# Performance work log

Measured on AMD Instinct MI355X. Metric: run time of the kernel, lower is better.

Reference implementation:

```python
import jax, jax.numpy as jnp
import numpy as np

N_EMBD = 2048
NUM_GROUPS = 8
EXPERTS_PER_GROUP = 8
ROUTER_TEMPERATURE = 1.0
N_TOKENS = 16384


def setup_inputs() -> dict:
    key = jax.random.key(0)
    kx, kg, ke = jax.random.split(key, 3)
    x = jax.random.normal(kx, (N_TOKENS, N_EMBD), dtype=jnp.float32)
    # nn.Linear(in, out, bias=False) stores weight as [out, in]; kaiming-uniform-ish scale
    bound = 1.0 / np.sqrt(N_EMBD)
    group_gate_w = jax.random.uniform(kg, (NUM_GROUPS, N_EMBD), dtype=jnp.float32,
                                      minval=-bound, maxval=bound)
    expert_gate_w = jax.random.uniform(ke, (NUM_GROUPS * EXPERTS_PER_GROUP, N_EMBD),
                                       dtype=jnp.float32, minval=-bound, maxval=bound)
    return {"x": x, "group_gate_w": group_gate_w, "expert_gate_w": expert_gate_w}


def reference(x, group_gate_w, expert_gate_w):
    N = x.shape[0]
    G = NUM_GROUPS
    E_g = EXPERTS_PER_GROUP
    inv_temp = 1.0 / ROUTER_TEMPERATURE

    # Level 1: group routing
    group_logits = jnp.einsum('nd,gd->ng', x, group_gate_w)            # [N, G]
    group_probs = jax.nn.softmax(group_logits * inv_temp, axis=-1)     # [N, G]
    group_mask = group_probs >= (1.0 / G)                              # [N, G]

    # Level 2: expert routing within each group
    expert_logits = jnp.einsum('nd,ed->ne', x, expert_gate_w)          # [N, G*E_g]
    expert_logits = expert_logits.reshape(N, G, E_g)
    expert_probs = jax.nn.softmax(expert_logits * inv_temp, axis=-1)   # [N, G, E_g]
    expert_mask = expert_probs >= (1.0 / E_g)                          # [N, G, E_g]

    valid_mask_3d = group_mask[:, :, None] & expert_mask               # [N, G, E_g]
    selected_weights_3d = (group_probs[:, :, None] * expert_probs) * valid_mask_3d.astype(x.dtype)

    valid_mask = valid_mask_3d.reshape(N, G * E_g)
    selected_weights = selected_weights_3d.reshape(N, G * E_g)
    weight_sum = jnp.clip(jnp.sum(selected_weights, axis=-1, keepdims=True), 1e-9, None)
    normalized_weights = selected_weights / weight_sum
    return (valid_mask, normalized_weights)
```

## Files before the change

### kernel.cpp

```cpp
#include <hip/hip_runtime.h>


#define NT 16384
#define NE 2048
#define NCHUNK 16
#define TOK 32
#define NTH 256
#define TILE 2048
#define BUFSZ 40960
#define LDS_BYTES 81920

typedef _Float16 v8h __attribute__((ext_vector_type(8)));
typedef float    v4f __attribute__((ext_vector_type(4)));

__global__ __launch_bounds__(NTH, 2)
void router(const float* __restrict__ x, const float* __restrict__ gw,
            const float* __restrict__ ew, float* __restrict__ out)
{
    __shared__ __align__(16) char sm[LDS_BYTES];
    const int tid  = threadIdx.x;
    const int lane = tid & 63;
    const int w    = tid >> 6;
    const int t0   = blockIdx.x * TOK;

    const float* wsrc[5]; int who[5]; int wz[5];
    #pragma unroll
    for (int i = 0; i < 5; ++i) {
        int s = tid + i * NTH;
        int gate = s >> 4, kslot = s & 15;
        int ks = kslot >> 2, q = kslot & 3;
        int m = gate & 15, g = gate >> 4;
        int swz = (q ^ (ks << 1)) & 7;
        who[i] = (g * 4 + ks) * TILE + (((q * 16 + m) ^ swz) << 4);
        if (gate < 64)      { wz[i] = 0; wsrc[i] = ew + (size_t)gate * NE + kslot * 8; }
        else if (gate < 72) { wz[i] = 0; wsrc[i] = gw + (size_t)(gate - 64) * NE + kslot * 8; }
        else                { wz[i] = 1; wsrc[i] = ew; }
    }

    const int tt = w >> 1, s2 = w & 1;
    const float* xp = x + (size_t)(t0 + tt * 16 + (lane & 15)) * NE + (lane >> 4) * 8;

    int rdk[2];
    #pragma unroll
    for (int ksl = 0; ksl < 2; ++ksl) {
        int ks = s2 * 2 + ksl;
        int swz = ((lane >> 4) ^ (ks << 1)) & 7;
        rdk[ksl] = ks * TILE + ((lane ^ swz) << 4);
    }

    float4 wr[5][2], xr[2][2];

    auto wload = [&](int c) {
        const int kc = c * 128;
        #pragma unroll
        for (int i = 0; i < 5; ++i) {
            if (!wz[i]) {
                wr[i][0] = *(const float4*)(wsrc[i] + kc);
                wr[i][1] = *(const float4*)(wsrc[i] + kc + 4);
            } else {
                wr[i][0] = make_float4(0.f, 0.f, 0.f, 0.f);
                wr[i][1] = make_float4(0.f, 0.f, 0.f, 0.f);
            }
        }
    };
    auto xload = [&](int c) {
        #pragma unroll
        for (int ksl = 0; ksl < 2; ++ksl) {
            const float* p = xp + c * 128 + (s2 * 2 + ksl) * 32;
            xr[ksl][0] = *(const float4*)(p);
            xr[ksl][1] = *(const float4*)(p + 4);
        }
    };
    auto split8 = [](const float4& a, const float4& b, v8h& h, v8h& l) {
        float v[8] = {a.x, a.y, a.z, a.w, b.x, b.y, b.z, b.w};
        #pragma unroll
        for (int j = 0; j < 8; ++j) {
            _Float16 hh = (_Float16)v[j];
            h[j] = hh;
            l[j] = (_Float16)((v[j] - (float)hh) * 2048.0f);
        }
    };
    auto wcommit = [&](int buf) {
        const int bb = buf * BUFSZ;
        #pragma unroll
        for (int i = 0; i < 5; ++i) {
            v8h h, l;
            split8(wr[i][0], wr[i][1], h, l);
            *(v8h*)(sm + bb + who[i])        = h;
            *(v8h*)(sm + bb + who[i] + 1024) = l;
        }
    };

    v4f accHH[5], accC[5];
    #pragma unroll
    for (int g = 0; g < 5; ++g) { accHH[g] = (v4f)(0.f); accC[g] = (v4f)(0.f); }

    wload(0); xload(0);
    wcommit(0);
    v8h Bh[2], Bl[2];
    for (int c = 0; c < NCHUNK; ++c) {
        #pragma unroll
        for (int ksl = 0; ksl < 2; ++ksl)
            split8(xr[ksl][0], xr[ksl][1], Bh[ksl], Bl[ksl]);
        if (c + 1 < NCHUNK) { xload(c + 1); wload(c + 1); }
        __syncthreads();
        const int bb = (c & 1) * BUFSZ;
        #pragma unroll
        for (int ksl = 0; ksl < 2; ++ksl) {
            #pragma unroll
            for (int g = 0; g < 5; ++g) {
                const char* ab = sm + bb + g * (4 * TILE) + rdk[ksl];
                v8h Ah = *(const v8h*)(ab);
                v8h Al = *(const v8h*)(ab + 1024);
                accHH[g] = __builtin_amdgcn_mfma_f32_16x16x32_f16(Ah, Bh[ksl], accHH[g], 0, 0, 0);
                accC[g]  = __builtin_amdgcn_mfma_f32_16x16x32_f16(Ah, Bl[ksl], accC[g], 0, 0, 0);
                accC[g]  = __builtin_amdgcn_mfma_f32_16x16x32_f16(Al, Bh[ksl], accC[g], 0, 0, 0);
            }
        }
        if (c + 1 < NCHUNK) wcommit((c + 1) & 1);
    }
    __syncthreads();

    float part[5][4];
    #pragma unroll
    for (int g = 0; g < 5; ++g)
        #pragma unroll
        for (int r = 0; r < 4; ++r)
            part[g][r] = accHH[g][r] + accC[g][r] * (1.0f / 2048.0f);

    float* red = (float*)sm;
    if (s2 == 1) {
        #pragma unroll
        for (int g = 0; g < 5; ++g)
            #pragma unroll
            for (int r = 0; r < 4; ++r)
                red[((tt * 5 + g) * 4 + r) * 64 + lane] = part[g][r];
    }
    __syncthreads();
    float* la = (float*)(sm + 10240);
    if (s2 == 0) {
        #pragma unroll
        for (int g = 0; g < 5; ++g)
            #pragma unroll
            for (int r = 0; r < 4; ++r) {
                float v = part[g][r] + red[((tt * 5 + g) * 4 + r) * 64 + lane];
                int gate  = g * 16 + (lane >> 4) * 4 + r;
                int token = tt * 16 + (lane & 15);
                la[token * 84 + gate] = v;
            }
    }
    __syncthreads();

    if (lane < 8) {
        const int token = w * 8 + lane;
        const float* lg = la + token * 84;
        float* M  = (float*)(sm + 20992) + token * 64;
        float* Wn = (float*)(sm + 29184) + token * 64;

        float gpb[8];
        float gmax = lg[64];
        #pragma unroll
        for (int g = 1; g < 8; ++g) gmax = fmaxf(gmax, lg[64 + g]);
        float gsum = 0.f;
        #pragma unroll
        for (int g = 0; g < 8; ++g) { gpb[g] = __expf(lg[64 + g] - gmax); gsum += gpb[g]; }
        const float ginv = 1.f / gsum;

        float sel[64];
        float wsum = 0.f;
        #pragma unroll
        for (int g = 0; g < 8; ++g) {
            const float gp_ = gpb[g] * ginv;
            float emax = lg[g * 8];
            #pragma unroll
            for (int j = 1; j < 8; ++j) emax = fmaxf(emax, lg[g * 8 + j]);
            float ep[8]; float esum = 0.f;
            #pragma unroll
            for (int j = 0; j < 8; ++j) { ep[j] = __expf(lg[g * 8 + j] - emax); esum += ep[j]; }
            const float einv = 1.f / esum;
            const bool gm = gp_ >= 0.125f;
            #pragma unroll
            for (int j = 0; j < 8; ++j) {
                const float pe = ep[j] * einv;
                const bool v = gm && (pe >= 0.125f);
                const float ww = v ? gp_ * pe : 0.f;
                M[g * 8 + j] = v ? 1.f : 0.f;
                sel[g * 8 + j] = ww;
                wsum += ww;
            }
        }
        const float inv = 1.f / fmaxf(wsum, 1e-9f);
        #pragma unroll
        for (int e = 0; e < 64; ++e) Wn[e] = sel[e] * inv;
    }
    __syncthreads();

    const float4* M4 = (const float4*)(sm + 20992);
    const float4* W4 = (const float4*)(sm + 29184);
    float4* o0 = (float4*)(out + (size_t)t0 * 64);
    float4* o1 = (float4*)(out + (size_t)NT * 64 + (size_t)t0 * 64);
    o0[tid]       = M4[tid];
    o0[tid + 256] = M4[tid + 256];
    o1[tid]       = W4[tid];
    o1[tid + 256] = W4[tid + 256];
}

extern "C" void kernel_launch(void* const* d_in, const int* in_sizes, int n_in,
                              void* d_out, int out_size, void* d_ws, size_t ws_size,
                              hipStream_t stream) {
    const float* x  = (const float*)d_in[0];
    const float* gw = (const float*)d_in[1];
    const float* ew = (const float*)d_in[2];
    float* out = (float*)d_out;
    (void)d_ws; (void)ws_size;

    router<<<dim3(NT / TOK), dim3(NTH), 0, stream>>>(x, gw, ew, out);
}
```

Baseline: 209.8 us.

## Pre-split gate weights to fp16 hi/lo in workspace and read them directly

Adds a prep kernel that converts the gate weights once per call into pre-swizzled fp16 hi/lo arrays in the workspace. The router then reads those fragments straight from global/L2 instead of staging them through double-buffered LDS with per-block conversion. The token tile is halved to 16 so 1024 blocks run, and all four waves split K, followed by a 4-way reduction. This removes the per-block weight conversion, the LDS traffic and the per-chunk barriers, at the cost of an extra launch and more repeated L2 reads of the weights.

```diff
diff --git a/kernel.cpp b/kernel.cpp
--- a/kernel.cpp
+++ b/kernel.cpp
@@ -3,159 +3,120 @@
 
 #define NT 16384
 #define NE 2048
-#define NCHUNK 16
-#define TOK 32
 #define NTH 256
-#define TILE 2048
-#define BUFSZ 40960
-#define LDS_BYTES 81920
+#define NBLK 1024
+#define WS_HALFS 163840
 
 typedef _Float16 v8h __attribute__((ext_vector_type(8)));
 typedef float    v4f __attribute__((ext_vector_type(4)));
 
-__global__ __launch_bounds__(NTH, 2)
-void router(const float* __restrict__ x, const float* __restrict__ gw,
-            const float* __restrict__ ew, float* __restrict__ out)
+__global__ __launch_bounds__(256, 1)
+void prep(const float* __restrict__ gw, const float* __restrict__ ew,
+          _Float16* __restrict__ wf)
 {
-    __shared__ __align__(16) char sm[LDS_BYTES];
+    const int f = blockIdx.x * 256 + threadIdx.x;
+    const int j  = f & 7;
+    const int sl = (f >> 3) & 63;
+    const int ks = (f >> 9) & 63;
+    const int g  = f >> 15;
+    const int q  = sl >> 4, m = sl & 15;
+    const int gate = g * 16 + m;
+    const int k = ks * 32 + q * 8 + j;
+    float v = 0.f;
+    if (gate < 64)      v = ew[gate * NE + k];
+    else if (gate < 72) v = gw[(gate - 64) * NE + k];
+    const _Float16 h = (_Float16)v;
+    wf[f]            = h;
+    wf[WS_HALFS + f] = (_Float16)((v - (float)h) * 2048.0f);
+}
+
+__global__ __launch_bounds__(NTH, 4)
+void router(const float* __restrict__ x, const _Float16* __restrict__ wf,
+            float* __restrict__ out)
+{
+    __shared__ __align__(16) char sm[20736];
     const int tid  = threadIdx.x;
     const int lane = tid & 63;
     const int w    = tid >> 6;
-    const int t0   = blockIdx.x * TOK;
+    const int t0   = blockIdx.x * 16;
 
-    const float* wsrc[5]; int who[5]; int wz[5];
+    const float* xp = x + (size_t)(t0 + (lane & 15)) * NE + (lane >> 4) * 8;
+
+    v4f accH[5], accC[5];
     #pragma unroll
-    for (int i = 0; i < 5; ++i) {
-        int s = tid + i * NTH;
-        int gate = s >> 4, kslot = s & 15;
-        int ks = kslot >> 2, q = kslot & 3;
-        int m = gate & 15, g = gate >> 4;
-        int swz = (q ^ (ks << 1)) & 7;
-        who[i] = (g * 4 + ks) * TILE + (((q * 16 + m) ^ swz) << 4);
-        if (gate < 64)      { wz[i] = 0; wsrc[i] = ew + (size_t)gate * NE + kslot * 8; }
-        else if (gate < 72) { wz[i] = 0; wsrc[i] = gw + (size_t)(gate - 64) * NE + kslot * 8; }
-        else                { wz[i] = 1; wsrc[i] = ew; }
-    }
+    for (int g = 0; g < 5; ++g) { accH[g] = (v4f)(0.f); accC[g] = (v4f)(0.f); }
 
-    const int tt = w >> 1, s2 = w & 1;
-    const float* xp = x + (size_t)(t0 + tt * 16 + (lane & 15)) * NE + (lane >> 4) * 8;
+    float4 xr0, xr1;
+    auto xload = [&](int s) {
+        const float* p = xp + (size_t)(w * 16 + s) * 32;
+        xr0 = *(const float4*)(p);
+        xr1 = *(const float4*)(p + 4);
+    };
 
-    int rdk[2];
-    #pragma unroll
-    for (int ksl = 0; ksl < 2; ++ksl) {
-        int ks = s2 * 2 + ksl;
-        int swz = ((lane >> 4) ^ (ks << 1)) & 7;
-        rdk[ksl] = ks * TILE + ((lane ^ swz) << 4);
-    }
-
-    float4 wr[5][2], xr[2][2];
-
-    auto wload = [&](int c) {
-        const int kc = c * 128;
-        #pragma unroll
-        for (int i = 0; i < 5; ++i) {
-            if (!wz[i]) {
-                wr[i][0] = *(const float4*)(wsrc[i] + kc);
-                wr[i][1] = *(const float4*)(wsrc[i] + kc + 4);
-            } else {
-                wr[i][0] = make_float4(0.f, 0.f, 0.f, 0.f);
-                wr[i][1] = make_float4(0.f, 0.f, 0.f, 0.f);
+    xload(0);
+    for (int s = 0; s < 16; ++s) {
+        v8h Bh, Bl;
+        {
+            const float xv[8] = {xr0.x, xr0.y, xr0.z, xr0.w, xr1.x, xr1.y, xr1.z, xr1.w};
+            #pragma unroll
+            for (int j = 0; j < 8; ++j) {
+                const _Float16 hh = (_Float16)xv[j];
+                Bh[j] = hh;
+                Bl[j] = (_Float16)((xv[j] - (float)hh) * 2048.0f);
             }
         }
-    };
-    auto xload = [&](int c) {
+        if (s + 1 < 16) xload(s + 1);
+
+        const int ks = w * 16 + s;
+        const _Float16* base = wf + ((size_t)ks * 64 + lane) * 8;
         #pragma unroll
-        for (int ksl = 0; ksl < 2; ++ksl) {
-            const float* p = xp + c * 128 + (s2 * 2 + ksl) * 32;
-            xr[ksl][0] = *(const float4*)(p);
-            xr[ksl][1] = *(const float4*)(p + 4);
+        for (int g = 0; g < 5; ++g) {
+            const v8h Ah = *(const v8h*)(base + g * 32768);
+            const v8h Al = *(const v8h*)(base + g * 32768 + WS_HALFS);
+            accH[g] = __builtin_amdgcn_mfma_f32_16x16x32_f16(Ah, Bh, accH[g], 0, 0, 0);
+            accC[g] = __builtin_amdgcn_mfma_f32_16x16x32_f16(Ah, Bl, accC[g], 0, 0, 0);
+            accC[g] = __builtin_amdgcn_mfma_f32_16x16x32_f16(Al, Bh, accC[g], 0, 0, 0);
         }
-    };
-    auto split8 = [](const float4& a, const float4& b, v8h& h, v8h& l) {
-        float v[8] = {a.x, a.y, a.z, a.w, b.x, b.y, b.z, b.w};
-        #pragma unroll
-        for (int j = 0; j < 8; ++j) {
-            _Float16 hh = (_Float16)v[j];
-            h[j] = hh;
-            l[j] = (_Float16)((v[j] - (float)hh) * 2048.0f);
-        }
-    };
-    auto wcommit = [&](int buf) {
-        const int bb = buf * BUFSZ;
-        #pragma unroll
-        for (int i = 0; i < 5; ++i) {
-            v8h h, l;
-            split8(wr[i][0], wr[i][1], h, l);
-            *(v8h*)(sm + bb + who[i])        = h;
-            *(v8h*)(sm + bb + who[i] + 1024) = l;
-        }
-    };
-
-    v4f accHH[5], accC[5];
-    #pragma unroll
-    for (int g = 0; g < 5; ++g) { accHH[g] = (v4f)(0.f); accC[g] = (v4f)(0.f); }
-
-    wload(0); xload(0);
-    wcommit(0);
-    v8h Bh[2], Bl[2];
-    for (int c = 0; c < NCHUNK; ++c) {
-        #pragma unroll
-        for (int ksl = 0; ksl < 2; ++ksl)
-            split8(xr[ksl][0], xr[ksl][1], Bh[ksl], Bl[ksl]);
-        if (c + 1 < NCHUNK) { xload(c + 1); wload(c + 1); }
-        __syncthreads();
-        const int bb = (c & 1) * BUFSZ;
-        #pragma unroll
-        for (int ksl = 0; ksl < 2; ++ksl) {
-            #pragma unroll
-            for (int g = 0; g < 5; ++g) {
-                const char* ab = sm + bb + g * (4 * TILE) + rdk[ksl];
-                v8h Ah = *(const v8h*)(ab);
-                v8h Al = *(const v8h*)(ab + 1024);
-                accHH[g] = __builtin_amdgcn_mfma_f32_16x16x32_f16(Ah, Bh[ksl], accHH[g], 0, 0, 0);
-                accC[g]  = __builtin_amdgcn_mfma_f32_16x16x32_f16(Ah, Bl[ksl], accC[g], 0, 0, 0);
-                accC[g]  = __builtin_amdgcn_mfma_f32_16x16x32_f16(Al, Bh[ksl], accC[g], 0, 0, 0);
-            }
-        }
-        if (c + 1 < NCHUNK) wcommit((c + 1) & 1);
     }
-    __syncthreads();
 
     float part[5][4];
     #pragma unroll
     for (int g = 0; g < 5; ++g)
         #pragma unroll
         for (int r = 0; r < 4; ++r)
-            part[g][r] = accHH[g][r] + accC[g][r] * (1.0f / 2048.0f);
+            part[g][r] = accH[g][r] + accC[g][r] * (1.0f / 2048.0f);
 
     float* red = (float*)sm;
-    if (s2 == 1) {
+    if (w > 0) {
         #pragma unroll
         for (int g = 0; g < 5; ++g)
             #pragma unroll
             for (int r = 0; r < 4; ++r)
-                red[((tt * 5 + g) * 4 + r) * 64 + lane] = part[g][r];
+                red[(((w - 1) * 5 + g) * 4 + r) * 64 + lane] = part[g][r];
     }
     __syncthreads();
-    float* la = (float*)(sm + 10240);
-    if (s2 == 0) {
+    float* la = (float*)(sm + 15360);
+    if (w == 0) {
         #pragma unroll
         for (int g = 0; g < 5; ++g)
             #pragma unroll
             for (int r = 0; r < 4; ++r) {
-                float v = part[g][r] + red[((tt * 5 + g) * 4 + r) * 64 + lane];
-                int gate  = g * 16 + (lane >> 4) * 4 + r;
-                int token = tt * 16 + (lane & 15);
+                float v = part[g][r]
+                        + red[((0 * 5 + g) * 4 + r) * 64 + lane]
+                        + red[((1 * 5 + g) * 4 + r) * 64 + lane]
+                        + red[((2 * 5 + g) * 4 + r) * 64 + lane];
+                const int gate  = g * 16 + (lane >> 4) * 4 + r;
+                const int token = lane & 15;
                 la[token * 84 + gate] = v;
             }
     }
     __syncthreads();
 
-    if (lane < 8) {
-        const int token = w * 8 + lane;
+    if (lane < 4) {
+        const int token = w * 4 + lane;
         const float* lg = la + token * 84;
-        float* M  = (float*)(sm + 20992) + token * 64;
-        float* Wn = (float*)(sm + 29184) + token * 64;
+        float* M  = (float*)sm + token * 64;
+        float* Wn = (float*)(sm + 4096) + token * 64;
 
         float gpb[8];
         float gmax = lg[64];
@@ -195,14 +156,12 @@
     }
     __syncthreads();
 
-    const float4* M4 = (const float4*)(sm + 20992);
-    const float4* W4 = (const float4*)(sm + 29184);
+    const float4* M4 = (const float4*)sm;
+    const float4* W4 = (const float4*)(sm + 4096);
     float4* o0 = (float4*)(out + (size_t)t0 * 64);
     float4* o1 = (float4*)(out + (size_t)NT * 64 + (size_t)t0 * 64);
-    o0[tid]       = M4[tid];
-    o0[tid + 256] = M4[tid + 256];
-    o1[tid]       = W4[tid];
-    o1[tid + 256] = W4[tid + 256];
+    o0[tid] = M4[tid];
+    o1[tid] = W4[tid];
 }
 
 extern "C" void kernel_launch(void* const* d_in, const int* in_sizes, int n_in,
@@ -212,7 +171,9 @@
     const float* gw = (const float*)d_in[1];
     const float* ew = (const float*)d_in[2];
     float* out = (float*)d_out;
-    (void)d_ws; (void)ws_size;
+    _Float16* wf = (_Float16*)d_ws;
+    (void)ws_size; (void)in_sizes; (void)n_in; (void)out_size;
 
-    router<<<dim3(NT / TOK), dim3(NTH), 0, stream>>>(x, gw, ew, out);
+    prep<<<dim3(640), dim3(256), 0, stream>>>(gw, ew, wf);
+    router<<<dim3(NBLK), dim3(NTH), 0, stream>>>(x, wf, out);
 }
```

Result: slower. 225.7 us (+7.6%).
